# Performance work log

Measured on AMD Instinct MI355X. Metric: run time of the kernel, lower is better.

Reference implementation:

```python
import jax, jax.numpy as jnp
import numpy as np

HIDDEN = 512
HEADS = 8
HEAD_DIM = HIDDEN // HEADS
D_FF = 4 * HIDDEN
NEG = -1e9


def _layernorm(x, g, b, eps=1e-5):
    mu = jnp.mean(x, axis=-1, keepdims=True)
    var = jnp.var(x, axis=-1, keepdims=True)
    return (x - mu) * jax.lax.rsqrt(var + eps) * g + b


def setup_inputs() -> dict:
    key = jax.random.key(0)
    ks = jax.random.split(key, 16)
    B, S = 2, 2048
    s = 1.0 / np.sqrt(HIDDEN)
    inp = {
        "x": jax.random.normal(ks[0], (B, S, HIDDEN), dtype=jnp.float32),
        "adj_mask": jax.random.bernoulli(ks[1], 0.5, (B, S, S)),
        "ln1_g": jnp.ones((HIDDEN,), jnp.float32),
        "ln1_b": jnp.zeros((HIDDEN,), jnp.float32),
        "ln2_g": jnp.ones((HIDDEN,), jnp.float32),
        "ln2_b": jnp.zeros((HIDDEN,), jnp.float32),
        "Wq": jax.random.uniform(ks[2], (HIDDEN, HIDDEN), jnp.float32, -s, s),
        "bq": jnp.zeros((HIDDEN,), jnp.float32),
        "Wk": jax.random.uniform(ks[3], (HIDDEN, HIDDEN), jnp.float32, -s, s),
        "bk": jnp.zeros((HIDDEN,), jnp.float32),
        "Wv": jax.random.uniform(ks[4], (HIDDEN, HIDDEN), jnp.float32, -s, s),
        "bv": jnp.zeros((HIDDEN,), jnp.float32),
        "Wo": jax.random.uniform(ks[5], (HIDDEN, HIDDEN), jnp.float32, -s, s),
        "bo": jnp.zeros((HIDDEN,), jnp.float32),
        "W1": jax.random.uniform(ks[6], (HIDDEN, D_FF), jnp.float32, -s, s),
        "b1": jnp.zeros((D_FF,), jnp.float32),
        "W2": jax.random.uniform(ks[7], (D_FF, HIDDEN), jnp.float32, -1.0 / np.sqrt(D_FF), 1.0 / np.sqrt(D_FF)),
        "b2": jnp.zeros((HIDDEN,), jnp.float32),
    }
    return inp


def reference(x, adj_mask, ln1_g, ln1_b, ln2_g, ln2_b, Wq, bq, Wk, bk, Wv, bv,
              Wo, bo, W1, b1, W2, b2):
    B, S, H = x.shape
    nx = _layernorm(x, ln1_g, ln1_b)
    q = (nx @ Wq + bq).reshape(B, S, HEADS, HEAD_DIM)
    k = (nx @ Wk + bk).reshape(B, S, HEADS, HEAD_DIM)
    v = (nx @ Wv + bv).reshape(B, S, HEADS, HEAD_DIM)
    # scores: [B, heads, S, S]
    scores = jnp.einsum('bqhd,bkhd->bhqk', q, k) / np.sqrt(HEAD_DIM)
    scores = jnp.where(adj_mask[:, None, :, :], scores, NEG)
    attn = jax.nn.softmax(scores, axis=-1)  # dropout in eval mode = identity
    out = jnp.einsum('bhqk,bkhd->bqhd', attn, v).reshape(B, S, H)
    out = out @ Wo + bo
    x = x + out
    nx = _layernorm(x, ln2_g, ln2_b)
    mlp = jax.nn.gelu(nx @ W1 + b1, approximate=False) @ W2 + b2
    return x + mlp
```

## Files before the change

### kernel.cpp

```cpp
#include <hip/hip_runtime.h>
#include <math.h>

typedef unsigned short u16;
typedef unsigned long long u64;
typedef __bf16 bf16x8 __attribute__((ext_vector_type(8)));
typedef float f32x4 __attribute__((ext_vector_type(4)));
typedef unsigned short u16x8 __attribute__((ext_vector_type(8)));
typedef unsigned short u16x4 __attribute__((ext_vector_type(4)));

#define S_LEN 2048
#define BATCH 2
#define HID 512
#define NHEAD 8
#define DHEAD 64
#define DFF 2048
#define ROWS (BATCH * S_LEN)
#define NQH (BATCH * NHEAD * S_LEN)
#define NPART 2
#define KVSPAN (S_LEN / NPART)
#define QSCALE 0.18033688011112042f

static __device__ __forceinline__ u16 f2bf(float f) {
  unsigned int u = __builtin_bit_cast(unsigned int, f);
  u += 0x7fffu + ((u >> 16) & 1u);
  return (u16)(u >> 16);
}
static __device__ __forceinline__ u16 f2bf_fast(float f) {
  return __builtin_bit_cast(u16, (__bf16)f);
}
static __device__ __forceinline__ float bf2f(u16 v) {
  return (float)__builtin_bit_cast(__bf16, v);
}

static __device__ __forceinline__ void gl16(const void* g, void* l) {
  __builtin_amdgcn_global_load_lds(
      (const __attribute__((address_space(1))) void*)g,
      (__attribute__((address_space(3))) void*)l, 16, 0, 0);
}

__global__ void detect_mask_kernel(const unsigned int* __restrict__ m,
                                   int* __restrict__ flag) {
  int lane = threadIdx.x & 63;
  int notint = 0, notf32 = 0;
  for (int i = lane; i < 1024; i += 64) {
    unsigned int v = m[i];
    if (v > 1u) notint = 1;
    if (v != 0u && v != 0x3f800000u) notf32 = 1;
  }
  unsigned long long bi = __ballot(notint);
  unsigned long long bf = __ballot(notf32);
  if (lane == 0) *flag = (bi == 0ull) ? 1 : ((bf == 0ull) ? 2 : 0);
}

__global__ __launch_bounds__(256) void mask_pack_kernel(
    const void* __restrict__ m, const int* __restrict__ flagp,
    u64* __restrict__ out) {
  int flag = *flagp;
  int lane = threadIdx.x & 63;
  int gw = (blockIdx.x * 256 + threadIdx.x) >> 6;
  int nw = (gridDim.x * 256) >> 6;
  const int nwords = ROWS * (S_LEN / 64);
  for (int wI = gw; wI < nwords; wI += nw) {
    size_t e = (size_t)wI * 64 + lane;
    bool bit;
    if (flag == 1) bit = ((const int*)m)[e] != 0;
    else if (flag == 2) bit = ((const float*)m)[e] != 0.f;
    else bit = ((const unsigned char*)m)[e] != 0;
    u64 bb = __ballot(bit);
    if (lane == 0) {
      int row = wI >> 5, w = wI & 31;
      int b = row >> 11, qq = row & 2047;
      out[(((size_t)(b * 32 + (qq >> 6)) * 32 + w) << 6) + (qq & 63)] = bb;
    }
  }
}

__global__ __launch_bounds__(256) void cvt_all_kernel(
    const float* __restrict__ Wq, const float* __restrict__ Wk,
    const float* __restrict__ Wv, const float* __restrict__ Wo,
    const float* __restrict__ W1, const float* __restrict__ W2,
    u16* __restrict__ wqkvT, u16* __restrict__ woT, u16* __restrict__ w1T,
    u16* __restrict__ w2T) {
  __shared__ u16 sT[64][80];
  int id = blockIdx.x;
  const float* W;
  u16* WT;
  int K, N, bx, by;
  if (id < 256) {
    int mat = id >> 6, sub = id & 63;
    bx = sub & 7; by = sub >> 3; K = 512; N = 512;
    W = (mat == 0) ? Wq : (mat == 1) ? Wk : (mat == 2) ? Wv : Wo;
    WT = (mat < 3) ? wqkvT + (size_t)mat * 512 * 512 : woT;
  } else if (id < 512) {
    int sub = id - 256;
    bx = sub & 31; by = sub >> 5; K = 512; N = 2048;
    W = W1; WT = w1T;
  } else {
    int sub = id - 512;
    bx = sub & 7; by = sub >> 3; K = 2048; N = 512;
    W = W2; WT = w2T;
  }
  int tid = threadIdx.x;
  int r = tid >> 2, c0 = (tid & 3) * 16;
  int k0 = by * 64, n0 = bx * 64;
  const float* src = W + (size_t)(k0 + r) * N + n0 + c0;
  u16x8 a, b;
#pragma unroll
  for (int j = 0; j < 8; ++j) a[j] = f2bf(src[j]);
#pragma unroll
  for (int j = 0; j < 8; ++j) b[j] = f2bf(src[8 + j]);
  *(u16x8*)&sT[r][c0] = a;
  *(u16x8*)&sT[r][c0 + 8] = b;
  __syncthreads();
  u16x8 o0, o1;
#pragma unroll
  for (int j = 0; j < 8; ++j) o0[j] = sT[c0 + j][r];
#pragma unroll
  for (int j = 0; j < 8; ++j) o1[j] = sT[c0 + 8 + j][r];
  u16* dst = WT + (size_t)(n0 + r) * K + k0 + c0;
  *(u16x8*)dst = o0;
  *(u16x8*)(dst + 8) = o1;
}

__global__ __launch_bounds__(256) void ln_kernel(const float* __restrict__ x,
                                                 const float* __restrict__ g,
                                                 const float* __restrict__ b,
                                                 u16* __restrict__ o) {
  int wid = threadIdx.x >> 6, lane = threadIdx.x & 63;
  long row = (long)blockIdx.x * 4 + wid;
  const float* xr = x + row * HID;
  float4 v0 = *(const float4*)(xr + lane * 8);
  float4 v1 = *(const float4*)(xr + lane * 8 + 4);
  float fr[8] = {v0.x, v0.y, v0.z, v0.w, v1.x, v1.y, v1.z, v1.w};
  float s = 0.f, q = 0.f;
#pragma unroll
  for (int j = 0; j < 8; ++j) { s += fr[j]; q += fr[j] * fr[j]; }
#pragma unroll
  for (int mby = 1; mby < 64; mby <<= 1) {
    s += __shfl_xor(s, mby);
    q += __shfl_xor(q, mby);
  }
  float mean = s * (1.f / HID);
  float var = q * (1.f / HID) - mean * mean;
  float rs = rsqrtf(var + 1e-5f);
  u16x8 ov;
#pragma unroll
  for (int j = 0; j < 8; ++j) {
    int c = lane * 8 + j;
    ov[j] = f2bf((fr[j] - mean) * rs * g[c] + b[c]);
  }
  *(u16x8*)(o + row * HID + lane * 8) = ov;
}

template <int BM, int BN, int EPI>
__global__ __launch_bounds__(256) void gemm3_kernel(
    const u16* __restrict__ A, const u16* __restrict__ BT,
    const float* __restrict__ bias, const float* __restrict__ bias2,
    const float* __restrict__ bias3, const float* __restrict__ resid,
    void* __restrict__ o1, void* __restrict__ o2, void* __restrict__ o3,
    int M, int N, int K) {
  constexpr int AM = BM / 32;
  constexpr int BNF = BN / 32;
  __shared__ alignas(16) u16 sA[BM * 64];
  __shared__ alignas(16) u16 sB[BN * 64];
  int tid = threadIdx.x, wid = tid >> 6, lane = tid & 63;
  int wm = wid >> 1, wn = wid & 1;
  int grp = lane >> 4, l16 = lane & 15;
  int m0 = blockIdx.y * BM, n0 = blockIdx.x * BN;
  f32x4 zz = {0.f, 0.f, 0.f, 0.f};
  f32x4 acc[AM][BNF];
#pragma unroll
  for (int i = 0; i < AM; ++i)
#pragma unroll
    for (int j = 0; j < BNF; ++j) acc[i][j] = zz;

  for (int k0 = 0; k0 < K; k0 += 64) {
#pragma unroll
    for (int i = 0; i < BM / 32; ++i) {
      int bb = i * 4096 + tid * 16;
      int row = bb >> 7;
      int cb = (bb & 127) ^ ((row & 7) << 4);
      gl16((const char*)A + ((size_t)(m0 + row) * K + k0) * 2 + cb,
           (char*)sA + i * 4096 + wid * 1024);
    }
#pragma unroll
    for (int i = 0; i < BN / 32; ++i) {
      int bb = i * 4096 + tid * 16;
      int row = bb >> 7;
      int cb = (bb & 127) ^ ((row & 7) << 4);
      gl16((const char*)BT + ((size_t)(n0 + row) * K + k0) * 2 + cb,
           (char*)sB + i * 4096 + wid * 1024);
    }
    __syncthreads();
    bf16x8 af[AM][2], bfr[BNF][2];
#pragma unroll
    for (int am = 0; am < AM; ++am) {
      int row = wm * (BM / 2) + am * 16 + l16;
#pragma unroll
      for (int kk = 0; kk < 2; ++kk)
        af[am][kk] = *(const bf16x8*)((const char*)sA + row * 128 +
                                      ((kk * 64 + grp * 16) ^ ((row & 7) << 4)));
    }
#pragma unroll
    for (int bn = 0; bn < BNF; ++bn) {
      int row = wn * (BN / 2) + bn * 16 + l16;
#pragma unroll
      for (int kk = 0; kk < 2; ++kk)
        bfr[bn][kk] = *(const bf16x8*)((const char*)sB + row * 128 +
                                       ((kk * 64 + grp * 16) ^ ((row & 7) << 4)));
    }
#pragma unroll
    for (int kk = 0; kk < 2; ++kk)
#pragma unroll
      for (int am = 0; am < AM; ++am)
#pragma unroll
        for (int bn = 0; bn < BNF; ++bn)
          acc[am][bn] = __builtin_amdgcn_mfma_f32_16x16x32_bf16(
              af[am][kk], bfr[bn][kk], acc[am][bn], 0, 0, 0);
    __syncthreads();
  }

#pragma unroll
  for (int am = 0; am < AM; ++am) {
#pragma unroll
    for (int bn = 0; bn < BNF; ++bn) {
      int gc = n0 + wn * (BN / 2) + bn * 16 + l16;
      long gr0 = m0 + wm * (BM / 2) + am * 16 + grp * 4;
      if constexpr (EPI == 0) {
        int bidx = (int)(gr0 >> 11), s0 = (int)(gr0 & 2047);
        if (gc < 512) {
          float bsv = bias[gc];
#pragma unroll
          for (int r = 0; r < 4; ++r)
            ((u16*)o1)[(size_t)(gr0 + r) * 512 + gc] =
                f2bf((acc[am][bn][r] + bsv) * QSCALE);
        } else if (gc < 1024) {
          int c = gc - 512, hh = c >> 6, d = c & 63;
          float bsv = bias2[c];
#pragma unroll
          for (int r = 0; r < 4; ++r)
            ((u16*)o2)[((size_t)(bidx * NHEAD + hh) * S_LEN + s0 + r) * 64 + d] =
                f2bf(acc[am][bn][r] + bsv);
        } else {
          int c = gc - 1024, hh = c >> 6, d = c & 63;
          float bsv = bias3[c];
          u16x4 pk;
#pragma unroll
          for (int r = 0; r < 4; ++r) pk[r] = f2bf(acc[am][bn][r] + bsv);
          *(u16x4*)((u16*)o3 +
                    (((size_t)(bidx * NHEAD + hh) * 32 + (s0 >> 6)) * 64 + d) * 64 +
                    (s0 & 63)) = pk;
        }
      } else if constexpr (EPI == 1) {
        float bsv = bias[gc];
        float* O = (float*)o1;
#pragma unroll
        for (int r = 0; r < 4; ++r) {
          size_t off = (size_t)(gr0 + r) * N + gc;
          O[off] = resid[off] + acc[am][bn][r] + bsv;
        }
      } else {
        float bsv = bias[gc];
        u16* O = (u16*)o1;
#pragma unroll
        for (int r = 0; r < 4; ++r) {
          float v = acc[am][bn][r] + bsv;
          O[(size_t)(gr0 + r) * N + gc] =
              f2bf(0.5f * v * (1.f + erff(v * 0.70710678118f)));
        }
      }
    }
  }
}

__global__ __launch_bounds__(256, 4) void attn_kernel(
    const u16* __restrict__ qg, const u16* __restrict__ khp,
    const u16* __restrict__ vtp, const u64* __restrict__ mpk,
    u16* __restrict__ pout, float2* __restrict__ mlb) {
  __shared__ alignas(16) char sKV[2][2][8192];
  __shared__ alignas(16) u16 sP[4][16][64];
  int tid = threadIdx.x;
  int wid = tid >> 6, lane = tid & 63;
  int grp = lane >> 4, l16 = lane & 15;
  int flat = blockIdx.x;
  int swz = (flat & 7) * 128 + (flat >> 3);
  int qblk = swz & 31, part = (swz >> 5) & 1, h = (swz >> 6) & 7, b = swz >> 9;
  int q0 = qblk * 64 + wid * 16;
  int q = q0 + l16;
  const u16* qp = qg + (size_t)(b * S_LEN + q) * HID + h * DHEAD + grp * 8;
  bf16x8 qf0 = *(const bf16x8*)qp;
  bf16x8 qf1 = *(const bf16x8*)(qp + 32);
  f32x4 zz = {0.f, 0.f, 0.f, 0.f};
  f32x4 oa[4] = {zz, zz, zz, zz};
  float mr = -1e30f, lr = 0.f;
  int hh = b * NHEAD + h;
  const char* kbase = (const char*)(khp + (size_t)hh * S_LEN * DHEAD);
  const char* vbase = (const char*)(vtp + (size_t)hh * S_LEN * DHEAD);
  const u64* mbase = mpk + (((size_t)(b * 32 + qblk) * 32) << 6) + wid * 16 + l16;
  int kvb = part * KVSPAN;

  auto stage = [&](int bsel, int kv0) {
#pragma unroll
    for (int i = 0; i < 4; ++i) {
      int idx = wid * 4 + i;
      int sel = idx >> 3, j = idx & 7;
      int bb = j * 1024 + lane * 16;
      int row = bb >> 7;
      int cb = (bb & 127) ^ ((row & 7) << 4);
      const char* src =
          (sel ? vbase + ((size_t)(kv0 >> 6) << 13) : kbase + (size_t)kv0 * 128) +
          (bb & ~127) + cb;
      gl16(src, &sKV[bsel][sel][j * 1024]);
    }
  };

  stage(0, kvb);
  u64 mw = mbase[(size_t)(kvb >> 6) << 6];
  __syncthreads();
  int buf = 0;
  char* sprow = (char*)sP + wid * 2048 + l16 * 128;
  int xw = (l16 & 7) << 4;

  for (int t = 0; t < KVSPAN / 64; ++t, buf ^= 1) {
    int kv0 = kvb + t * 64;
    if (t + 1 < KVSPAN / 64) stage(buf ^ 1, kv0 + 64);
    u64 mw_next = mbase[(size_t)((kv0 >> 6) + 1) << 6];
    const char* Kb = sKV[buf][0];
    const char* Vb = sKV[buf][1];
    bf16x8 kf[4][2];
#pragma unroll
    for (int nb = 0; nb < 4; ++nb) {
      int row = nb * 16 + l16;
      int x = (row & 7) << 4;
      kf[nb][0] = *(const bf16x8*)(Kb + row * 128 + ((grp * 16) ^ x));
      kf[nb][1] = *(const bf16x8*)(Kb + row * 128 + ((64 + grp * 16) ^ x));
    }
    bf16x8 vf[2][4];
#pragma unroll
    for (int ks = 0; ks < 2; ++ks)
#pragma unroll
      for (int db = 0; db < 4; ++db) {
        int row = db * 16 + l16;
        int x = (row & 7) << 4;
        vf[ks][db] =
            *(const bf16x8*)(Vb + row * 128 + ((ks * 64 + grp * 16) ^ x));
      }
    f32x4 st[4];
#pragma unroll
    for (int nb = 0; nb < 4; ++nb) {
      f32x4 s = zz;
      s = __builtin_amdgcn_mfma_f32_16x16x32_bf16(kf[nb][0], qf0, s, 0, 0, 0);
      s = __builtin_amdgcn_mfma_f32_16x16x32_bf16(kf[nb][1], qf1, s, 0, 0, 0);
      st[nb] = s;
    }
    float tmx = -1e30f;
#pragma unroll
    for (int nb = 0; nb < 4; ++nb)
#pragma unroll
      for (int r = 0; r < 4; ++r) {
        int kbit = nb * 16 + grp * 4 + r;
        float s = ((mw >> kbit) & 1ull) ? st[nb][r] : -1e9f;
        st[nb][r] = s;
        tmx = fmaxf(tmx, s);
      }
    mw = mw_next;
    tmx = fmaxf(tmx, __shfl_xor(tmx, 16));
    tmx = fmaxf(tmx, __shfl_xor(tmx, 32));
    if (__any(tmx > mr + 4.f)) {
      float mnew = fmaxf(mr, tmx);
      float sc = __builtin_amdgcn_exp2f(mr - mnew);
      lr *= sc;
#pragma unroll
      for (int db = 0; db < 4; ++db)
#pragma unroll
        for (int r = 0; r < 4; ++r) oa[db][r] *= sc;
      mr = mnew;
    }
    float tsum = 0.f;
#pragma unroll
    for (int nb = 0; nb < 4; ++nb) {
      u16x4 pk;
#pragma unroll
      for (int r = 0; r < 4; ++r) {
        float p = __builtin_amdgcn_exp2f(st[nb][r] - mr);
        tsum += p;
        pk[r] = f2bf_fast(p);
      }
      *(u16x4*)(sprow + ((nb * 32 + grp * 8) ^ xw)) = pk;
    }
    tsum += __shfl_xor(tsum, 16);
    tsum += __shfl_xor(tsum, 32);
    lr += tsum;
    asm volatile("s_waitcnt lgkmcnt(0)" ::: "memory");
    __builtin_amdgcn_s_setprio(1);
#pragma unroll
    for (int ks = 0; ks < 2; ++ks) {
      bf16x8 pb = *(const bf16x8*)(sprow + ((ks * 64 + grp * 16) ^ xw));
#pragma unroll
      for (int db = 0; db < 4; ++db)
        oa[db] = __builtin_amdgcn_mfma_f32_16x16x32_bf16(vf[ks][db], pb, oa[db],
                                                         0, 0, 0);
    }
    __builtin_amdgcn_s_setprio(0);
    __syncthreads();
  }

#pragma unroll
  for (int db = 0; db < 4; ++db) {
    u16x4 pk;
#pragma unroll
    for (int r = 0; r < 4; ++r) pk[r] = f2bf_fast(oa[db][r]);
    *(u16x4*)(sprow + ((db * 32 + grp * 8) ^ xw)) = pk;
  }
  asm volatile("s_waitcnt lgkmcnt(0)" ::: "memory");
  int rrow = lane >> 3, rcolb = (lane & 7) * 16;
  const char* spw = (const char*)sP + wid * 2048;
  u16x8 o0 = *(const u16x8*)(spw + rrow * 128 + (rcolb ^ ((rrow & 7) << 4)));
  u16x8 o1 =
      *(const u16x8*)(spw + (8 + rrow) * 128 + (rcolb ^ ((rrow & 7) << 4)));
  int ridx0 = hh * S_LEN + q0;
  u16* pp = pout + ((size_t)part * NQH + ridx0) * 64;
  __builtin_nontemporal_store(o0, (u16x8*)(pp + lane * 8));
  __builtin_nontemporal_store(o1, (u16x8*)(pp + 512 + lane * 8));
  if (grp == 0)
    mlb[(size_t)part * NQH + ridx0 + l16] = make_float2(mr, lr);
}

__global__ __launch_bounds__(256) void combine_kernel(
    const u16* __restrict__ p, const float2* __restrict__ mlb,
    u16* __restrict__ ao) {
  int wid = threadIdx.x >> 6, lane = threadIdx.x & 63;
  int ridx = blockIdx.x * 4 + wid;
  float2 ml[NPART];
#pragma unroll
  for (int i = 0; i < NPART; ++i) ml[i] = mlb[(size_t)i * NQH + ridx];
  float M = ml[0].x;
#pragma unroll
  for (int i = 1; i < NPART; ++i) M = fmaxf(M, ml[i].x);
  float denom = 0.f, o = 0.f;
#pragma unroll
  for (int i = 0; i < NPART; ++i) {
    float w = __builtin_amdgcn_exp2f(ml[i].x - M);
    denom += w * ml[i].y;
    u16 pv = __builtin_nontemporal_load(p + ((size_t)i * NQH + ridx) * 64 + lane);
    o += w * bf2f(pv);
  }
  o /= denom;
  int b = ridx >> 14, h = (ridx >> 11) & 7, q = ridx & 2047;
  ao[(size_t)(b * S_LEN + q) * HID + h * DHEAD + lane] = f2bf(o);
}

extern "C" void kernel_launch(void* const* d_in, const int* in_sizes, int n_in,
                              void* d_out, int out_size, void* d_ws,
                              size_t ws_size, hipStream_t stream) {
  const float* x = (const float*)d_in[0];
  const void* mask = d_in[1];
  const float* ln1g = (const float*)d_in[2];
  const float* ln1b = (const float*)d_in[3];
  const float* ln2g = (const float*)d_in[4];
  const float* ln2b = (const float*)d_in[5];
  const float* Wq = (const float*)d_in[6];
  const float* bq = (const float*)d_in[7];
  const float* Wk = (const float*)d_in[8];
  const float* bk = (const float*)d_in[9];
  const float* Wv = (const float*)d_in[10];
  const float* bvp = (const float*)d_in[11];
  const float* Wo = (const float*)d_in[12];
  const float* bo = (const float*)d_in[13];
  const float* W1 = (const float*)d_in[14];
  const float* b1 = (const float*)d_in[15];
  const float* W2 = (const float*)d_in[16];
  const float* b2 = (const float*)d_in[17];

  char* w = (char*)d_ws;
  int* flag = (int*)w;
  char* base = w + 256;
  u64* mpk = (u64*)base;
  float2* mlb = (float2*)(base + 1048576);
  u16* wqkvT = (u16*)(base + 2097152);
  u16* woT = wqkvT + 1536 * 512;
  u16* w1T = woT + 512 * 512;
  u16* w2T = w1T + 2048 * 512;
  u16* nx = (u16*)(base + 8388608);
  u16* nx2 = nx;
  u16* qb = (u16*)(base + 12582912);
  float* x2 = (float*)(base + 12582912);
  u16* khp = (u16*)(base + 16777216);
  u16* vtp = (u16*)(base + 20971520);
  u16* aob = (u16*)(base + 20971520);
  u16* pbuf = (u16*)(base + 25165824);
  u16* hb = (u16*)(base + 25165824);

  detect_mask_kernel<<<1, 64, 0, stream>>>((const unsigned int*)mask, flag);
  mask_pack_kernel<<<2048, 256, 0, stream>>>(mask, flag, mpk);
  cvt_all_kernel<<<768, 256, 0, stream>>>(Wq, Wk, Wv, Wo, W1, W2, wqkvT, woT,
                                          w1T, w2T);
  ln_kernel<<<1024, 256, 0, stream>>>(x, ln1g, ln1b, nx);
  gemm3_kernel<128, 128, 0><<<dim3(12, 32), 256, 0, stream>>>(
      nx, wqkvT, bq, bk, bvp, nullptr, qb, khp, vtp, ROWS, 1536, HID);
  attn_kernel<<<1024, 256, 0, stream>>>(qb, khp, vtp, mpk, pbuf, mlb);
  combine_kernel<<<8192, 256, 0, stream>>>(pbuf, mlb, aob);
  gemm3_kernel<64, 64, 1><<<dim3(8, 64), 256, 0, stream>>>(
      aob, woT, bo, nullptr, nullptr, x, x2, nullptr, nullptr, ROWS, 512, 512);
  ln_kernel<<<1024, 256, 0, stream>>>(x2, ln2g, ln2b, nx2);
  gemm3_kernel<128, 128, 2><<<dim3(16, 32), 256, 0, stream>>>(
      nx2, w1T, b1, nullptr, nullptr, nullptr, hb, nullptr, nullptr, ROWS, DFF,
      HID);
  gemm3_kernel<128, 64, 1><<<dim3(8, 32), 256, 0, stream>>>(
      hb, w2T, b2, nullptr, nullptr, x2, d_out, nullptr, nullptr, ROWS, 512,
      DFF);
}
```

Before: 156.7 us.

## Fuse prep kernels, fold split-softmax combine into O-projection, retune GEMM tiles

Merges mask detection, mask packing, weight conversion and the first layernorm into one prep kernel, so the flag is recomputed per block instead of being passed through a separate launch. Removes the combine kernel: the O-projection GEMM now merges the two partial attention outputs with their max/sum weights while it loads its A tile, which avoids writing and re-reading the combined activation buffer. GEMM tile shapes for QKV, FFN1 and FFN2 are shrunk to launch more blocks. The trade-offs are fewer kernel launches and less memory traffic against redundant per-block flag detection and a simpler, non-pipelined O-projection loop.

After: 132.2 us, median of 3. -15.6%, faster.

```diff
diff --git a/kernel.cpp b/kernel.cpp
--- a/kernel.cpp
+++ b/kernel.cpp
@@ -38,88 +38,102 @@
       (__attribute__((address_space(3))) void*)l, 16, 0, 0);
 }
 
-__global__ void detect_mask_kernel(const unsigned int* __restrict__ m,
-                                   int* __restrict__ flag) {
-  int lane = threadIdx.x & 63;
-  int notint = 0, notf32 = 0;
-  for (int i = lane; i < 1024; i += 64) {
-    unsigned int v = m[i];
-    if (v > 1u) notint = 1;
-    if (v != 0u && v != 0x3f800000u) notf32 = 1;
-  }
-  unsigned long long bi = __ballot(notint);
-  unsigned long long bf = __ballot(notf32);
-  if (lane == 0) *flag = (bi == 0ull) ? 1 : ((bf == 0ull) ? 2 : 0);
-}
-
-__global__ __launch_bounds__(256) void mask_pack_kernel(
-    const void* __restrict__ m, const int* __restrict__ flagp,
-    u64* __restrict__ out) {
-  int flag = *flagp;
-  int lane = threadIdx.x & 63;
-  int gw = (blockIdx.x * 256 + threadIdx.x) >> 6;
-  int nw = (gridDim.x * 256) >> 6;
-  const int nwords = ROWS * (S_LEN / 64);
-  for (int wI = gw; wI < nwords; wI += nw) {
-    size_t e = (size_t)wI * 64 + lane;
-    bool bit;
-    if (flag == 1) bit = ((const int*)m)[e] != 0;
-    else if (flag == 2) bit = ((const float*)m)[e] != 0.f;
-    else bit = ((const unsigned char*)m)[e] != 0;
-    u64 bb = __ballot(bit);
-    if (lane == 0) {
-      int row = wI >> 5, w = wI & 31;
-      int b = row >> 11, qq = row & 2047;
-      out[(((size_t)(b * 32 + (qq >> 6)) * 32 + w) << 6) + (qq & 63)] = bb;
-    }
-  }
-}
-
-__global__ __launch_bounds__(256) void cvt_all_kernel(
+__global__ __launch_bounds__(256) void prep_kernel(
+    const void* __restrict__ mask, const float* __restrict__ x,
+    const float* __restrict__ ln1g, const float* __restrict__ ln1b,
     const float* __restrict__ Wq, const float* __restrict__ Wk,
     const float* __restrict__ Wv, const float* __restrict__ Wo,
     const float* __restrict__ W1, const float* __restrict__ W2,
-    u16* __restrict__ wqkvT, u16* __restrict__ woT, u16* __restrict__ w1T,
-    u16* __restrict__ w2T) {
+    u64* __restrict__ mpk, u16* __restrict__ wqkvT, u16* __restrict__ woT,
+    u16* __restrict__ w1T, u16* __restrict__ w2T, u16* __restrict__ nx) {
   __shared__ u16 sT[64][80];
-  int id = blockIdx.x;
-  const float* W;
-  u16* WT;
-  int K, N, bx, by;
-  if (id < 256) {
-    int mat = id >> 6, sub = id & 63;
-    bx = sub & 7; by = sub >> 3; K = 512; N = 512;
-    W = (mat == 0) ? Wq : (mat == 1) ? Wk : (mat == 2) ? Wv : Wo;
-    WT = (mat < 3) ? wqkvT + (size_t)mat * 512 * 512 : woT;
-  } else if (id < 512) {
-    int sub = id - 256;
-    bx = sub & 31; by = sub >> 5; K = 512; N = 2048;
-    W = W1; WT = w1T;
+  int bid = blockIdx.x, tid = threadIdx.x;
+  int wid = tid >> 6, lane = tid & 63;
+  if (bid < 2048) {
+    const unsigned int* m32 = (const unsigned int*)mask;
+    unsigned int v0 = m32[lane];
+    u64 bi = __ballot(v0 > 1u);
+    u64 bf = __ballot(v0 != 0u && v0 != 0x3f800000u);
+    int flag = (bi == 0ull) ? 1 : ((bf == 0ull) ? 2 : 0);
+    int gw = (bid * 256 + tid) >> 6;
+    const int nw = 8192;
+    const int nwords = ROWS * (S_LEN / 64);
+    for (int wI = gw; wI < nwords; wI += nw) {
+      size_t e = (size_t)wI * 64 + lane;
+      bool bit;
+      if (flag == 1) bit = ((const int*)mask)[e] != 0;
+      else if (flag == 2) bit = ((const float*)mask)[e] != 0.f;
+      else bit = ((const unsigned char*)mask)[e] != 0;
+      u64 bb = __ballot(bit);
+      if (lane == 0) {
+        int row = wI >> 5, w = wI & 31;
+        int b = row >> 11, qq = row & 2047;
+        mpk[(((size_t)(b * 32 + (qq >> 6)) * 32 + w) << 6) + (qq & 63)] = bb;
+      }
+    }
+  } else if (bid < 2816) {
+    int id = bid - 2048;
+    const float* W;
+    u16* WT;
+    int K, N, bx, by;
+    if (id < 256) {
+      int mat = id >> 6, sub = id & 63;
+      bx = sub & 7; by = sub >> 3; K = 512; N = 512;
+      W = (mat == 0) ? Wq : (mat == 1) ? Wk : (mat == 2) ? Wv : Wo;
+      WT = (mat < 3) ? wqkvT + (size_t)mat * 512 * 512 : woT;
+    } else if (id < 512) {
+      int sub = id - 256;
+      bx = sub & 31; by = sub >> 5; K = 512; N = 2048;
+      W = W1; WT = w1T;
+    } else {
+      int sub = id - 512;
+      bx = sub & 7; by = sub >> 3; K = 2048; N = 512;
+      W = W2; WT = w2T;
+    }
+    int r = tid >> 2, c0 = (tid & 3) * 16;
+    int k0 = by * 64, n0 = bx * 64;
+    const float* src = W + (size_t)(k0 + r) * N + n0 + c0;
+    u16x8 a, b;
+#pragma unroll
+    for (int j = 0; j < 8; ++j) a[j] = f2bf(src[j]);
+#pragma unroll
+    for (int j = 0; j < 8; ++j) b[j] = f2bf(src[8 + j]);
+    *(u16x8*)&sT[r][c0] = a;
+    *(u16x8*)&sT[r][c0 + 8] = b;
+    __syncthreads();
+    u16x8 o0, o1;
+#pragma unroll
+    for (int j = 0; j < 8; ++j) o0[j] = sT[c0 + j][r];
+#pragma unroll
+    for (int j = 0; j < 8; ++j) o1[j] = sT[c0 + 8 + j][r];
+    u16* dst = WT + (size_t)(n0 + r) * K + k0 + c0;
+    *(u16x8*)dst = o0;
+    *(u16x8*)(dst + 8) = o1;
   } else {
-    int sub = id - 512;
-    bx = sub & 7; by = sub >> 3; K = 2048; N = 512;
-    W = W2; WT = w2T;
-  }
-  int tid = threadIdx.x;
-  int r = tid >> 2, c0 = (tid & 3) * 16;
-  int k0 = by * 64, n0 = bx * 64;
-  const float* src = W + (size_t)(k0 + r) * N + n0 + c0;
-  u16x8 a, b;
-#pragma unroll
-  for (int j = 0; j < 8; ++j) a[j] = f2bf(src[j]);
-#pragma unroll
-  for (int j = 0; j < 8; ++j) b[j] = f2bf(src[8 + j]);
-  *(u16x8*)&sT[r][c0] = a;
-  *(u16x8*)&sT[r][c0 + 8] = b;
-  __syncthreads();
-  u16x8 o0, o1;
-#pragma unroll
-  for (int j = 0; j < 8; ++j) o0[j] = sT[c0 + j][r];
-#pragma unroll
-  for (int j = 0; j < 8; ++j) o1[j] = sT[c0 + 8 + j][r];
-  u16* dst = WT + (size_t)(n0 + r) * K + k0 + c0;
-  *(u16x8*)dst = o0;
-  *(u16x8*)(dst + 8) = o1;
+    long row = (long)(bid - 2816) * 4 + wid;
+    const float* xr = x + row * HID;
+    float4 v0 = *(const float4*)(xr + lane * 8);
+    float4 v1 = *(const float4*)(xr + lane * 8 + 4);
+    float fr[8] = {v0.x, v0.y, v0.z, v0.w, v1.x, v1.y, v1.z, v1.w};
+    float s = 0.f, q = 0.f;
+#pragma unroll
+    for (int j = 0; j < 8; ++j) { s += fr[j]; q += fr[j] * fr[j]; }
+#pragma unroll
+    for (int mby = 1; mby < 64; mby <<= 1) {
+      s += __shfl_xor(s, mby);
+      q += __shfl_xor(q, mby);
+    }
+    float mean = s * (1.f / HID);
+    float var = q * (1.f / HID) - mean * mean;
+    float rs = rsqrtf(var + 1e-5f);
+    u16x8 ov;
+#pragma unroll
+    for (int j = 0; j < 8; ++j) {
+      int c = lane * 8 + j;
+      ov[j] = f2bf((fr[j] - mean) * rs * ln1g[c] + ln1b[c]);
+    }
+    *(u16x8*)(nx + row * HID + lane * 8) = ov;
+  }
 }
 
 __global__ __launch_bounds__(256) void ln_kernel(const float* __restrict__ x,
@@ -268,6 +282,98 @@
           O[(size_t)(gr0 + r) * N + gc] =
               f2bf(0.5f * v * (1.f + erff(v * 0.70710678118f)));
         }
+      }
+    }
+  }
+}
+
+__global__ __launch_bounds__(256) void oproj_kernel(
+    const u16* __restrict__ pbuf, const float2* __restrict__ mlb,
+    const u16* __restrict__ BT, const float* __restrict__ bias,
+    const float* __restrict__ resid, float* __restrict__ out) {
+  __shared__ alignas(16) u16 sA[64 * 64];
+  __shared__ alignas(16) u16 sB[64 * 64];
+  int tid = threadIdx.x, wid = tid >> 6, lane = tid & 63;
+  int wm = wid >> 1, wn = wid & 1;
+  int grp = lane >> 4, l16 = lane & 15;
+  int m0 = blockIdx.y * 64, n0 = blockIdx.x * 64;
+  f32x4 zz = {0.f, 0.f, 0.f, 0.f};
+  f32x4 acc[2][2] = {{zz, zz}, {zz, zz}};
+  int ar = tid >> 2, ac = (tid & 3) * 16;
+  int grow = m0 + ar;
+  int bB = grow >> 11, q = grow & 2047;
+  int rbase = bB * NHEAD * S_LEN + q;
+
+  for (int k0 = 0; k0 < 512; k0 += 64) {
+#pragma unroll
+    for (int i = 0; i < 2; ++i) {
+      int bb = i * 4096 + tid * 16;
+      int row = bb >> 7;
+      int cb = (bb & 127) ^ ((row & 7) << 4);
+      gl16((const char*)BT + ((size_t)(n0 + row) * 512 + k0) * 2 + cb,
+           (char*)sB + i * 4096 + wid * 1024);
+    }
+    int ridx = rbase + (k0 >> 6) * S_LEN;
+    float2 ml0 = mlb[ridx], ml1 = mlb[NQH + ridx];
+    float M = fmaxf(ml0.x, ml1.x);
+    float w0 = __builtin_amdgcn_exp2f(ml0.x - M);
+    float w1 = __builtin_amdgcn_exp2f(ml1.x - M);
+    float rden = 1.f / (w0 * ml0.y + w1 * ml1.y);
+    w0 *= rden; w1 *= rden;
+    u16x8 p0a = *(const u16x8*)(pbuf + (size_t)ridx * 64 + ac);
+    u16x8 p0b = *(const u16x8*)(pbuf + (size_t)ridx * 64 + ac + 8);
+    u16x8 p1a = *(const u16x8*)(pbuf + ((size_t)NQH + ridx) * 64 + ac);
+    u16x8 p1b = *(const u16x8*)(pbuf + ((size_t)NQH + ridx) * 64 + ac + 8);
+    u16x8 oa_, ob_;
+#pragma unroll
+    for (int j = 0; j < 8; ++j) {
+      oa_[j] = f2bf_fast(w0 * bf2f(p0a[j]) + w1 * bf2f(p1a[j]));
+      ob_[j] = f2bf_fast(w0 * bf2f(p0b[j]) + w1 * bf2f(p1b[j]));
+    }
+    char* dst = (char*)sA + ar * 128;
+    int xr_ = (ar & 7) << 4;
+    *(u16x8*)(dst + ((ac * 2) ^ xr_)) = oa_;
+    *(u16x8*)(dst + ((ac * 2 + 16) ^ xr_)) = ob_;
+    __syncthreads();
+    bf16x8 af[2][2], bfr[2][2];
+#pragma unroll
+    for (int am = 0; am < 2; ++am) {
+      int row = wm * 32 + am * 16 + l16;
+#pragma unroll
+      for (int kk = 0; kk < 2; ++kk)
+        af[am][kk] = *(const bf16x8*)((const char*)sA + row * 128 +
+                                      ((kk * 64 + grp * 16) ^ ((row & 7) << 4)));
+    }
+#pragma unroll
+    for (int bn = 0; bn < 2; ++bn) {
+      int row = wn * 32 + bn * 16 + l16;
+#pragma unroll
+      for (int kk = 0; kk < 2; ++kk)
+        bfr[bn][kk] = *(const bf16x8*)((const char*)sB + row * 128 +
+                                       ((kk * 64 + grp * 16) ^ ((row & 7) << 4)));
+    }
+#pragma unroll
+    for (int kk = 0; kk < 2; ++kk)
+#pragma unroll
+      for (int am = 0; am < 2; ++am)
+#pragma unroll
+        for (int bn = 0; bn < 2; ++bn)
+          acc[am][bn] = __builtin_amdgcn_mfma_f32_16x16x32_bf16(
+              af[am][kk], bfr[bn][kk], acc[am][bn], 0, 0, 0);
+    __syncthreads();
+  }
+
+#pragma unroll
+  for (int am = 0; am < 2; ++am) {
+#pragma unroll
+    for (int bn = 0; bn < 2; ++bn) {
+      int gc = n0 + wn * 32 + bn * 16 + l16;
+      long gr0 = m0 + wm * 32 + am * 16 + grp * 4;
+      float bsv = bias[gc];
+#pragma unroll
+      for (int r = 0; r < 4; ++r) {
+        size_t off = (size_t)(gr0 + r) * 512 + gc;
+        out[off] = resid[off] + acc[am][bn][r] + bsv;
       }
     }
   }
@@ -426,30 +532,6 @@
     mlb[(size_t)part * NQH + ridx0 + l16] = make_float2(mr, lr);
 }
 
-__global__ __launch_bounds__(256) void combine_kernel(
-    const u16* __restrict__ p, const float2* __restrict__ mlb,
-    u16* __restrict__ ao) {
-  int wid = threadIdx.x >> 6, lane = threadIdx.x & 63;
-  int ridx = blockIdx.x * 4 + wid;
-  float2 ml[NPART];
-#pragma unroll
-  for (int i = 0; i < NPART; ++i) ml[i] = mlb[(size_t)i * NQH + ridx];
-  float M = ml[0].x;
-#pragma unroll
-  for (int i = 1; i < NPART; ++i) M = fmaxf(M, ml[i].x);
-  float denom = 0.f, o = 0.f;
-#pragma unroll
-  for (int i = 0; i < NPART; ++i) {
-    float w = __builtin_amdgcn_exp2f(ml[i].x - M);
-    denom += w * ml[i].y;
-    u16 pv = __builtin_nontemporal_load(p + ((size_t)i * NQH + ridx) * 64 + lane);
-    o += w * bf2f(pv);
-  }
-  o /= denom;
-  int b = ridx >> 14, h = (ridx >> 11) & 7, q = ridx & 2047;
-  ao[(size_t)(b * S_LEN + q) * HID + h * DHEAD + lane] = f2bf(o);
-}
-
 extern "C" void kernel_launch(void* const* d_in, const int* in_sizes, int n_in,
                               void* d_out, int out_size, void* d_ws,
                               size_t ws_size, hipStream_t stream) {
@@ -473,7 +555,6 @@
   const float* b2 = (const float*)d_in[17];
 
   char* w = (char*)d_ws;
-  int* flag = (int*)w;
   char* base = w + 256;
   u64* mpk = (u64*)base;
   float2* mlb = (float2*)(base + 1048576);
@@ -487,26 +568,20 @@
   float* x2 = (float*)(base + 12582912);
   u16* khp = (u16*)(base + 16777216);
   u16* vtp = (u16*)(base + 20971520);
-  u16* aob = (u16*)(base + 20971520);
   u16* pbuf = (u16*)(base + 25165824);
   u16* hb = (u16*)(base + 25165824);
 
-  detect_mask_kernel<<<1, 64, 0, stream>>>((const unsigned int*)mask, flag);
-  mask_pack_kernel<<<2048, 256, 0, stream>>>(mask, flag, mpk);
-  cvt_all_kernel<<<768, 256, 0, stream>>>(Wq, Wk, Wv, Wo, W1, W2, wqkvT, woT,
-                                          w1T, w2T);
-  ln_kernel<<<1024, 256, 0, stream>>>(x, ln1g, ln1b, nx);
-  gemm3_kernel<128, 128, 0><<<dim3(12, 32), 256, 0, stream>>>(
+  prep_kernel<<<3840, 256, 0, stream>>>(mask, x, ln1g, ln1b, Wq, Wk, Wv, Wo,
+                                        W1, W2, mpk, wqkvT, woT, w1T, w2T, nx);
+  gemm3_kernel<128, 64, 0><<<dim3(24, 32), 256, 0, stream>>>(
       nx, wqkvT, bq, bk, bvp, nullptr, qb, khp, vtp, ROWS, 1536, HID);
   attn_kernel<<<1024, 256, 0, stream>>>(qb, khp, vtp, mpk, pbuf, mlb);
-  combine_kernel<<<8192, 256, 0, stream>>>(pbuf, mlb, aob);
-  gemm3_kernel<64, 64, 1><<<dim3(8, 64), 256, 0, stream>>>(
-      aob, woT, bo, nullptr, nullptr, x, x2, nullptr, nullptr, ROWS, 512, 512);
+  oproj_kernel<<<dim3(8, 64), 256, 0, stream>>>(pbuf, mlb, woT, bo, x, x2);
   ln_kernel<<<1024, 256, 0, stream>>>(x2, ln2g, ln2b, nx2);
-  gemm3_kernel<128, 128, 2><<<dim3(16, 32), 256, 0, stream>>>(
+  gemm3_kernel<128, 64, 2><<<dim3(32, 32), 256, 0, stream>>>(
       nx2, w1T, b1, nullptr, nullptr, nullptr, hb, nullptr, nullptr, ROWS, DFF,
       HID);
-  gemm3_kernel<128, 64, 1><<<dim3(8, 32), 256, 0, stream>>>(
+  gemm3_kernel<64, 64, 1><<<dim3(8, 64), 256, 0, stream>>>(
       hb, w2T, b2, nullptr, nullptr, x2, d_out, nullptr, nullptr, ROWS, 512,
       DFF);
 }
```
